# Kernel tuning notes

Measured on AMD Instinct MI355X. Metric: run time of the kernel, lower is better.

The kernel has to match this reference:

```python
import jax, jax.numpy as jnp
import numpy as np
import math

B, S, D = 2, 1024, 2048
NH, NKV, HD = 16, 8, 128
NREP = NH // NKV
WINDOW = 256  # = max_seq_len; ReRoPE window


def _rope(x, cos, sin):
    # x: (b, s, h, d); cos/sin broadcastable to (b, s, h, d//2). Interleaved pairs (llama2.c style).
    b, s, h, d = x.shape
    xr, xi = x[..., ::2], x[..., 1::2]
    or_ = xr * cos - xi * sin
    oi = xr * sin + xi * cos
    return jnp.stack([or_, oi], axis=-1).reshape(b, s, h, d)


def setup_inputs() -> dict:
    key = jax.random.key(0)
    kx, kq, kk, kv, ko = jax.random.split(key, 5)
    # real RoPE tables (theta=10000), per-position, half head dim
    inv = 1.0 / (10000.0 ** (np.arange(0, HD, 2, dtype=np.float32) / HD))
    fr = np.outer(np.arange(S, dtype=np.float32), inv).astype(np.float32)  # (S, HD//2)
    sc = 0.02
    return {
        "x": jax.random.normal(kx, (B, S, D), jnp.float32),
        "freqs_cos": jnp.asarray(np.cos(fr)),
        "freqs_sin": jnp.asarray(np.sin(fr)),
        "wq": jax.random.normal(kq, (D, NH * HD), jnp.float32) * sc,
        "wk": jax.random.normal(kk, (D, NKV * HD), jnp.float32) * sc,
        "wv": jax.random.normal(kv, (D, NKV * HD), jnp.float32) * sc,
        "wo": jax.random.normal(ko, (NH * HD, D), jnp.float32) * sc,
    }


def reference(x, freqs_cos, freqs_sin, wq, wk, wv, wo):
    b, s, _ = x.shape
    xq = (x @ wq).reshape(b, s, NH, HD)
    xk = (x @ wk).reshape(b, s, NKV, HD)
    xv = (x @ wv).reshape(b, s, NKV, HD)

    cos = freqs_cos[:s][None, :, None, :]
    sin = freqs_sin[:s][None, :, None, :]
    q1 = _rope(xq, cos, sin)   # standard RoPE
    k1 = _rope(xk, cos, sin)

    # ReRoPE: queries rotated at the fixed clamp position = window; keys unrotated
    cw = freqs_cos[WINDOW][None, None, None, :]
    sw = freqs_sin[WINDOW][None, None, None, :]
    q2 = _rope(xq, cw, sw)
    k2 = xk

    rep = lambda a: jnp.repeat(a, NREP, axis=2)          # repeat_kv (GQA)
    heads = lambda a: a.transpose(0, 2, 1, 3)            # (b, h, s, d)
    q1, k1, v = heads(q1), heads(rep(k1)), heads(rep(xv))
    q2, k2 = heads(q2), heads(rep(k2))

    scale = 1.0 / math.sqrt(HD)
    s1 = jnp.einsum("bhqd,bhkd->bhqk", q1, k1) * scale
    s2 = jnp.einsum("bhqd,bhkd->bhqk", q2, k2) * scale

    i = jnp.arange(s)[:, None]
    j = jnp.arange(s)[None, :]
    causal = j <= i
    rect = causal & (j > i - WINDOW)                     # rectified_mask band
    scores = jnp.where(rect, s1, s2)
    scores = jnp.where(causal, scores, -jnp.inf)         # mask_inf (causal)

    attn = jax.nn.softmax(scores.astype(jnp.float32), axis=-1).astype(x.dtype)
    out = jnp.einsum("bhqk,bhkd->bhqd", attn, v)
    out = out.transpose(0, 2, 1, 3).reshape(b, s, NH * HD)
    return out @ wo
```

## Files before the change

kernel.cpp:

```cpp
#include <hip/hip_runtime.h>
#include <hip/hip_bf16.h>

#define BDIM 2
#define SDIM 1024
#define DDIM 2048
#define NH 16
#define NKV 8
#define HD 128
#define WINDOW 256

typedef __bf16 bf16;
typedef __bf16 bf16x4 __attribute__((ext_vector_type(4)));
typedef __bf16 bf16x8 __attribute__((ext_vector_type(8)));
typedef float f32x4 __attribute__((ext_vector_type(4)));

#define L2E 1.44269504088896341f

__device__ inline bf16x8 load8(const bf16* p) { return *reinterpret_cast<const bf16x8*>(p); }

__device__ __forceinline__ void gl_lds16(const bf16* g, bf16* l) {
  __builtin_amdgcn_global_load_lds(
      (__attribute__((address_space(1))) void*)g,
      (__attribute__((address_space(3))) void*)l,
      16, 0, 0);
}

__global__ __launch_bounds__(256) void prep(const float* __restrict__ x,
                                            const float* __restrict__ wq,
                                            const float* __restrict__ wk,
                                            const float* __restrict__ wv,
                                            const float* __restrict__ wo,
                                            bf16* __restrict__ xb,
                                            bf16* __restrict__ wqkvT,
                                            bf16* __restrict__ woT) {
  __shared__ bf16 tile[32][33];
  int z = blockIdx.z;
  int tx = threadIdx.x, ty = threadIdx.y;
  if (z == 4) {
    long i = (((long)blockIdx.y * 64 + blockIdx.x) * 256 + ty * 32 + tx) * 4;
    float4 a = *(const float4*)(x + i);
    bf16x4 o;
    o[0] = (bf16)a.x; o[1] = (bf16)a.y; o[2] = (bf16)a.z; o[3] = (bf16)a.w;
    *(bf16x4*)(xb + i) = o;
    return;
  }
  const float* src; bf16* dst; int C;
  if (z == 0)      { src = wq; dst = wqkvT;                 C = 2048; }
  else if (z == 1) { src = wk; dst = wqkvT + 2048L * 2048;  C = 1024; }
  else if (z == 2) { src = wv; dst = wqkvT + 3072L * 2048;  C = 1024; }
  else             { src = wo; dst = woT;                   C = 2048; }
  int c0 = blockIdx.x * 32, r0 = blockIdx.y * 32;
  if (c0 >= C) return;
  for (int yy = ty; yy < 32; yy += 8)
    tile[yy][tx] = (bf16)src[(long)(r0 + yy) * C + c0 + tx];
  __syncthreads();
  for (int yy = ty; yy < 32; yy += 8)
    dst[(long)(c0 + yy) * 2048 + r0 + tx] = tile[tx][yy];
}

#define BK 64
__global__ __launch_bounds__(256) void gemm_bt_n64(const bf16* __restrict__ A,
                                                   const bf16* __restrict__ Bt,
                                                   float* __restrict__ C,
                                                   int M, int N, int K) {
  __shared__ bf16 smem[2 * 12288];
  int t = threadIdx.x;
  int wid = t >> 6, lane = t & 63;
  int wm = (wid >> 1) * 64, wn = (wid & 1) * 32;
  int fm = lane & 15, quad = lane >> 4;

  int wg = blockIdx.y * 32 + blockIdx.x;
  int swz = (wg & 7) * 64 + (wg >> 3);
  int by = swz >> 5, bx = swz & 31;
  int m0 = by * 128, n0 = bx * 64;

  const bf16* Ag = A + (long)m0 * K;
  const bf16* Bg = Bt + (long)n0 * K;

  f32x4 acc[4][2] = {};

  auto stA = [&](bf16* dst, int k0, int p) {
    int idx = p * 256 + t;
    int row = idx >> 3, ccs = idx & 7;
    int gcol = ((ccs ^ (row & 7)) * 8);
    gl_lds16(&Ag[(long)row * K + k0 + gcol], &dst[idx * 8]);
  };
  auto stB = [&](bf16* dst, int k0, int p) {
    int idx = p * 256 + t;
    int row = idx >> 3, ccs = idx & 7;
    int gcol = ((ccs ^ (row & 7)) * 8);
    gl_lds16(&Bg[(long)row * K + k0 + gcol], &dst[idx * 8]);
  };
  auto cmp = [&](const bf16* As, const bf16* Bs, int ks) {
    int cc = (ks >> 3) + quad;
    bf16x8 af[4], bfr[2];
    for (int i = 0; i < 4; ++i) {
      int fr = wm + i * 16 + fm;
      af[i] = load8(&As[(fr * 8 + (cc ^ (fr & 7))) * 8]);
    }
    for (int j = 0; j < 2; ++j) {
      int fr = wn + j * 16 + fm;
      bfr[j] = load8(&Bs[(fr * 8 + (cc ^ (fr & 7))) * 8]);
    }
    __builtin_amdgcn_s_setprio(1);
    for (int i = 0; i < 4; ++i)
      for (int j = 0; j < 2; ++j)
        acc[i][j] = __builtin_amdgcn_mfma_f32_16x16x32_bf16(af[i], bfr[j], acc[i][j], 0, 0, 0);
    __builtin_amdgcn_s_setprio(0);
  };

  {
    bf16* As = smem; bf16* Bs = smem + 8192;
    stA(As, 0, 0); stA(As, 0, 1); stA(As, 0, 2); stA(As, 0, 3);
    stB(Bs, 0, 0); stB(Bs, 0, 1);
  }
  const int NT = K / BK;
  for (int kt = 0; kt < NT; ++kt) {
    int cur = kt & 1;
    bf16* As = smem + cur * 12288;
    bf16* Bs = As + 8192;
    if (kt + 1 < NT) {
      bf16* An = smem + (cur ^ 1) * 12288;
      bf16* Bn = An + 8192;
      int kn = (kt + 1) * BK;
      stA(An, kn, 0); stA(An, kn, 1); stB(Bn, kn, 0);
      asm volatile("s_waitcnt vmcnt(3)\n\ts_barrier" ::: "memory");
      cmp(As, Bs, 0);
      stA(An, kn, 2); stA(An, kn, 3); stB(Bn, kn, 1);
      cmp(As, Bs, 32);
      asm volatile("s_barrier" ::: "memory");
    } else {
      asm volatile("s_waitcnt vmcnt(0)\n\ts_barrier" ::: "memory");
      cmp(As, Bs, 0);
      cmp(As, Bs, 32);
    }
  }
  for (int i = 0; i < 4; ++i)
    for (int r = 0; r < 4; ++r) {
      int row = m0 + wm + i * 16 + quad * 4 + r;
      for (int j = 0; j < 2; ++j) {
        int col = n0 + wn + j * 16 + fm;
        C[(long)row * N + col] = acc[i][j][r];
      }
    }
}

#define VPITCH 130
__global__ __launch_bounds__(512) void gemm_qkv(const bf16* __restrict__ A,
                                                const bf16* __restrict__ Bt,
                                                const float* __restrict__ fc,
                                                const float* __restrict__ fs,
                                                bf16* __restrict__ q0,
                                                bf16* __restrict__ k1,
                                                bf16* __restrict__ k2,
                                                bf16* __restrict__ vT) {
  const int K = 2048;
  __shared__ bf16 smem[2 * 24576];
  int t = threadIdx.x;
  int wid = t >> 6, lane = t & 63;
  int wm = (wid >> 2) * 64, wn = (wid & 3) * 64;
  int fm = lane & 15, quad = lane >> 4;

  int wg = blockIdx.y * 16 + blockIdx.x;
  int swz = (wg & 7) * 32 + (wg >> 3);
  int by = swz >> 4, bx = swz & 15;
  int m0 = by * 128, n0 = bx * 256;

  const bf16* Ag = A + (long)m0 * K;
  const bf16* Bg = Bt + (long)n0 * K;

  f32x4 acc[4][4] = {};

  auto stA = [&](bf16* dst, int k0, int p) {
    int idx = p * 512 + t;
    int row = idx >> 3, ccs = idx & 7;
    int gcol = ((ccs ^ (row & 7)) * 8);
    gl_lds16(&Ag[(long)row * K + k0 + gcol], &dst[idx * 8]);
  };
  auto stB = [&](bf16* dst, int k0, int p) {
    int idx = p * 512 + t;
    int row = idx >> 3, ccs = idx & 7;
    int gcol = ((ccs ^ (row & 7)) * 8);
    gl_lds16(&Bg[(long)row * K + k0 + gcol], &dst[idx * 8]);
  };
  auto cmp = [&](const bf16* As, const bf16* Bs, int ks) {
    int cc = (ks >> 3) + quad;
    bf16x8 af[4], bfr[4];
    for (int i = 0; i < 4; ++i) {
      int fr = wm + i * 16 + fm;
      af[i] = load8(&As[(fr * 8 + (cc ^ (fr & 7))) * 8]);
    }
    for (int j = 0; j < 4; ++j) {
      int fr = wn + j * 16 + fm;
      bfr[j] = load8(&Bs[(fr * 8 + (cc ^ (fr & 7))) * 8]);
    }
    __builtin_amdgcn_s_setprio(1);
    for (int i = 0; i < 4; ++i)
      for (int j = 0; j < 4; ++j)
        acc[i][j] = __builtin_amdgcn_mfma_f32_16x16x32_bf16(af[i], bfr[j], acc[i][j], 0, 0, 0);
    __builtin_amdgcn_s_setprio(0);
  };

  {
    bf16* As = smem; bf16* Bs = smem + 8192;
    stA(As, 0, 0); stA(As, 0, 1);
    stB(Bs, 0, 0); stB(Bs, 0, 1); stB(Bs, 0, 2); stB(Bs, 0, 3);
  }
  const int NT = K / 64;
  for (int kt = 0; kt < NT; ++kt) {
    int cur = kt & 1;
    bf16* As = smem + cur * 24576;
    bf16* Bs = As + 8192;
    if (kt + 1 < NT) {
      bf16* An = smem + (cur ^ 1) * 24576;
      bf16* Bn = An + 8192;
      int kn = (kt + 1) * 64;
      stA(An, kn, 0); stA(An, kn, 1); stB(Bn, kn, 0);
      asm volatile("s_waitcnt vmcnt(3)\n\ts_barrier" ::: "memory");
      cmp(As, Bs, 0);
      stB(Bn, kn, 1); stB(Bn, kn, 2); stB(Bn, kn, 3);
      cmp(As, Bs, 32);
      asm volatile("s_barrier" ::: "memory");
    } else {
      asm volatile("s_waitcnt vmcnt(0)\n\ts_barrier" ::: "memory");
      cmp(As, Bs, 0);
      cmp(As, Bs, 32);
    }
  }

  if (n0 < 2048) {
    const float scale = 0.08838834764831845f;
    for (int i = 0; i < 4; ++i)
      for (int r = 0; r < 4; ++r) {
        int row = m0 + wm + i * 16 + quad * 4 + r;
        for (int j = 0; j < 4; ++j) {
          int gc = n0 + wn + j * 16 + fm;
          q0[(long)row * 2048 + gc] = (bf16)(acc[i][j][r] * scale);
        }
      }
  } else if (n0 < 3072) {
    float sgn = (lane & 1) ? 1.f : -1.f;
    float cwj[4], swj[4];
    for (int j = 0; j < 4; ++j) {
      int dp = ((wn + j * 16 + fm) & 127) >> 1;
      cwj[j] = fc[WINDOW * 64 + dp];
      swj[j] = fs[WINDOW * 64 + dp] * (-sgn);
    }
    for (int i = 0; i < 4; ++i)
      for (int r = 0; r < 4; ++r) {
        int row = m0 + wm + i * 16 + quad * 4 + r;
        int s = row & (SDIM - 1);
        for (int j = 0; j < 4; ++j) {
          int kc = n0 - 2048 + wn + j * 16 + fm;
          int dp = (kc & 127) >> 1;
          float v = acc[i][j][r];
          float pp = __shfl_xor(v, 1, 64);
          float c = fc[s * 64 + dp];
          float sn = fs[s * 64 + dp] * sgn;
          long dst = (long)row * 1024 + kc;
          k1[dst] = (bf16)(v * c + pp * sn);
          k2[dst] = (bf16)(v * cwj[j] + pp * swj[j]);
        }
      }
  } else {
    int vv0 = (n0 - 3072) >> 7;
    int s0l = m0 & (SDIM - 1);
    int bq = m0 >> 10;
    for (int half = 0; half < 2; ++half) {
      __syncthreads();
      if (((wn >> 7) & 1) == half) {
        for (int i = 0; i < 4; ++i)
          for (int j = 0; j < 4; ++j) {
            int col = (wn & 127) + j * 16 + fm;
            for (int r = 0; r < 4; ++r) {
              int rl = wm + i * 16 + quad * 4 + r;
              smem[col * VPITCH + rl] = (bf16)acc[i][j][r];
            }
          }
      }
      __syncthreads();
      bf16* vtg = vT + ((long)(bq * NKV + vv0 + half)) * 128 * 1024;
      for (int p = 0; p < 4; ++p) {
        int c = p * 512 + t;
        int d = c >> 4, sc = (c & 15) * 8;
        *(bf16x8*)&vtg[(long)d * 1024 + s0l + sc] = *(bf16x8*)&smem[d * VPITCH + sc];
      }
    }
  }
}

__global__ __launch_bounds__(512) void attn_kernel(const bf16* __restrict__ q0,
                                                   const bf16* __restrict__ k1,
                                                   const bf16* __restrict__ k2,
                                                   const bf16* __restrict__ vT,
                                                   const float* __restrict__ fc,
                                                   const float* __restrict__ fs,
                                                   bf16* __restrict__ aout) {
  __shared__ bf16 Kb[3][8192];
  __shared__ bf16 Vb[3][8192];
  __shared__ bf16 Pl[8][16][72];
  __shared__ float stats[8][16];

  int kvh = blockIdx.y;
  int b = blockIdx.z;
  int tile = b ? (15 - blockIdx.x) : blockIdx.x;
  int t = threadIdx.x;
  int w = t >> 6, lane = t & 63;
  int wl = w & 3;
  int h = kvh * 2 + (w >> 2);
  int m = lane & 15, quad = lane >> 4;

  const bf16* k1g0 = k1 + ((long)b * SDIM) * 1024 + kvh * 128;
  const bf16* k2g0 = k2 + ((long)b * SDIM) * 1024 + kvh * 128;
  const bf16* vtg0 = vT + ((long)(b * NKV + kvh)) * 128 * 1024;

  int t0 = tile * 64;
  int i0w = t0 + wl * 16;
  int i = i0w + m;

  const bf16* q0p = q0 + ((long)(b * SDIM + i0w + m)) * 2048 + h * 128 + quad * 8;
  bf16x8 q0f[4], q1f[4];
  for (int kc = 0; kc < 4; ++kc) {
    q0f[kc] = load8(q0p + kc * 32);
    for (int p4 = 0; p4 < 4; ++p4) {
      int dp = kc * 16 + quad * 4 + p4;
      float c = fc[i * 64 + dp], sn = fs[i * 64 + dp];
      float xr = (float)q0f[kc][2 * p4], xi = (float)q0f[kc][2 * p4 + 1];
      q1f[kc][2 * p4]     = (bf16)(xr * c - xi * sn);
      q1f[kc][2 * p4 + 1] = (bf16)(xr * sn + xi * c);
    }
  }

  int NS2 = tile >= 4 ? tile - 3 : 0;
  int NSEG = NS2 + (tile < 4 ? tile + 1 : 5);
  int j1base = tile >= 4 ? t0 - 256 : 0;

  auto segj = [&](int s, int& j0, int& md) {
    if (s < NS2) { j0 = s * 64; md = 2; } else { j0 = j1base + (s - NS2) * 64; md = 1; }
  };
  auto stage = [&](int s) {
    int j0, md; segj(s, j0, md);
    const bf16* kg0 = (md == 1) ? k1g0 : k2g0;
    bf16* Kd = Kb[s % 3];
    bf16* Vd = Vb[s % 3];
    for (int p = 0; p < 2; ++p) {
      int idx = p * 512 + t;
      int kr = idx >> 4, kcs = idx & 15;
      int kg = (kcs ^ (kr & 15)) * 8;
      gl_lds16(&kg0[(long)(j0 + kr) * 1024 + kg], &Kd[idx * 8]);
      int vd = idx >> 3, vcs = idx & 7;
      int vg = (vcs ^ (vd & 7)) * 8;
      gl_lds16(&vtg0[(long)vd * 1024 + j0 + vg], &Vd[idx * 8]);
    }
  };

  f32x4 o[8] = {};
  float mrow = -INFINITY, lrow = 0.f;

  stage(0);
  if (NSEG > 1) stage(1);

  for (int s = 0; s < NSEG; ++s) {
    if (s + 2 < NSEG) {
      stage(s + 2);
      asm volatile("s_waitcnt vmcnt(8)\n\ts_barrier" ::: "memory");
    } else if (s + 1 < NSEG) {
      asm volatile("s_waitcnt vmcnt(4)\n\ts_barrier" ::: "memory");
    } else {
      asm volatile("s_waitcnt vmcnt(0)\n\ts_barrier" ::: "memory");
    }

    int j0, md; segj(s, j0, md);
    bool fullseg = (md == 2) && (s < NS2 - 1);
    const bf16* Ks = Kb[s % 3];
    const bf16* VTs = Vb[s % 3];

    f32x4 sc[4] = {};
    __builtin_amdgcn_s_setprio(1);
    if (md == 1) {
      for (int st = 0; st < 4; ++st)
        for (int kc = 0; kc < 4; ++kc) {
          int cc = kc * 4 + quad;
          sc[st] = __builtin_amdgcn_mfma_f32_16x16x32_bf16(
              load8(&Ks[((st * 16 + m) * 16 + (cc ^ m)) * 8]), q1f[kc], sc[st], 0, 0, 0);
        }
    } else {
      for (int st = 0; st < 4; ++st)
        for (int kc = 0; kc < 4; ++kc) {
          int cc = kc * 4 + quad;
          sc[st] = __builtin_amdgcn_mfma_f32_16x16x32_bf16(
              load8(&Ks[((st * 16 + m) * 16 + (cc ^ m)) * 8]), q0f[kc], sc[st], 0, 0, 0);
        }
    }
    __builtin_amdgcn_s_setprio(0);

    float sv[4][4];
    for (int st = 0; st < 4; ++st)
      for (int r = 0; r < 4; ++r) {
        float v = sc[st][r];
        if (!fullseg) {
          int j = j0 + st * 16 + quad * 4 + r;
          if (md == 1) {
            if (j > i || j <= i - WINDOW) v = -INFINITY;
          } else {
            if (j > i - WINDOW) v = -INFINITY;
          }
        }
        sv[st][r] = v;
      }

    float bm = -INFINITY;
    for (int st = 0; st < 4; ++st)
      for (int r = 0; r < 4; ++r) bm = fmaxf(bm, sv[st][r]);
    bm = fmaxf(bm, __shfl_xor(bm, 16, 64));
    bm = fmaxf(bm, __shfl_xor(bm, 32, 64));
    float mnew = fmaxf(mrow, bm);
    float rs = 0.f;
    for (int st = 0; st < 4; ++st) {
      bf16x4 pk;
      for (int r = 0; r < 4; ++r) {
        float pvv = exp2f((sv[st][r] - mnew) * L2E);
        rs += pvv;
        pk[r] = (bf16)pvv;
      }
      *(bf16x4*)&Pl[w][m][st * 16 + quad * 4] = pk;
    }
    rs += __shfl_xor(rs, 16, 64);
    rs += __shfl_xor(rs, 32, 64);
    if (__any(mnew > mrow)) {
      float alpha = exp2f((mrow - mnew) * L2E);
      lrow = lrow * alpha + rs;
      mrow = mnew;
      if (lane < 16) stats[w][lane] = alpha;
      f32x4 av = *(f32x4*)&stats[w][quad * 4];
      for (int n8 = 0; n8 < 8; ++n8)
        for (int r = 0; r < 4; ++r) o[n8][r] *= av[r];
    } else {
      lrow += rs;
    }

    for (int kc = 0; kc < 2; ++kc) {
      bf16x8 af = load8(&Pl[w][m][kc * 32 + quad * 8]);
      int cc = kc * 4 + quad;
      __builtin_amdgcn_s_setprio(1);
      for (int n8 = 0; n8 < 8; ++n8) {
        int d = n8 * 16 + m;
        o[n8] = __builtin_amdgcn_mfma_f32_16x16x32_bf16(
            af, load8(&VTs[(d * 8 + (cc ^ (d & 7))) * 8]), o[n8], 0, 0, 0);
      }
      __builtin_amdgcn_s_setprio(0);
    }
    asm volatile("s_barrier" ::: "memory");
  }

  if (lane < 16) stats[w][lane] = lrow;
  __builtin_amdgcn_s_waitcnt(0);
  f32x4 lv = *(f32x4*)&stats[w][quad * 4];
  for (int n8 = 0; n8 < 8; ++n8)
    for (int r = 0; r < 4; ++r) {
      int row = i0w + quad * 4 + r;
      float val = o[n8][r] / lv[r];
      aout[((long)(b * SDIM + row)) * 2048 + h * 128 + n8 * 16 + m] = (bf16)val;
    }
}

extern "C" void kernel_launch(void* const* d_in, const int* in_sizes, int n_in,
                              void* d_out, int out_size, void* d_ws, size_t ws_size,
                              hipStream_t stream) {
  const float* x  = (const float*)d_in[0];
  const float* fc = (const float*)d_in[1];
  const float* fs = (const float*)d_in[2];
  const float* wq = (const float*)d_in[3];
  const float* wk = (const float*)d_in[4];
  const float* wv = (const float*)d_in[5];
  const float* wo = (const float*)d_in[6];
  float* out = (float*)d_out;

  bf16* wqkvT = (bf16*)d_ws;
  bf16* woT   = wqkvT + 4096L * 2048;
  bf16* xb    = woT + 2048L * 2048;
  bf16* q0b   = xb + 2048L * 2048;
  bf16* k1b   = q0b + 2048L * 2048;
  bf16* k2b   = k1b + 2048L * 1024;
  bf16* vT    = k2b + 2048L * 1024;
  bf16* aout  = vT + 2048L * 1024;

  prep<<<dim3(64, 64, 5), dim3(32, 8), 0, stream>>>(x, wq, wk, wv, wo, xb, wqkvT, woT);

  gemm_qkv<<<dim3(16, 16), 512, 0, stream>>>(xb, wqkvT, fc, fs, q0b, k1b, k2b, vT);

  attn_kernel<<<dim3(16, 8, 2), 512, 0, stream>>>(q0b, k1b, k2b, vT, fc, fs, aout);

  gemm_bt_n64<<<dim3(32, 16), 256, 0, stream>>>(aout, woT, out, 2048, 2048, 2048);
}
```

Measured before the change: 229.1 us.

## Restructure attention into 128-thread blocks with two query subtiles per wave

The attention kernel now runs 512 blocks of 2 waves, one wave per query head of the GQA pair. Each block covers 32 query rows, so each wave handles two 16-row subtiles that share the K and V fragment loads. The K/V pipeline drops from triple to double buffering, with a single barrier per segment. The mask-free segment test now also covers interior window segments. The aim is more blocks for better CU occupancy and load balance, plus more MFMA work per LDS load. The cost is more total K/V global traffic, because each 32-row tile restages its segments, and more register pressure from the doubled accumulators.

```diff
diff --git a/kernel.cpp b/kernel.cpp
--- a/kernel.cpp
+++ b/kernel.cpp
@@ -289,178 +289,227 @@
   }
 }
 
-__global__ __launch_bounds__(512) void attn_kernel(const bf16* __restrict__ q0,
+__global__ __launch_bounds__(128) void attn_kernel(const bf16* __restrict__ q0,
                                                    const bf16* __restrict__ k1,
                                                    const bf16* __restrict__ k2,
                                                    const bf16* __restrict__ vT,
                                                    const float* __restrict__ fc,
                                                    const float* __restrict__ fs,
                                                    bf16* __restrict__ aout) {
-  __shared__ bf16 Kb[3][8192];
-  __shared__ bf16 Vb[3][8192];
-  __shared__ bf16 Pl[8][16][72];
-  __shared__ float stats[8][16];
-
-  int kvh = blockIdx.y;
-  int b = blockIdx.z;
-  int tile = b ? (15 - blockIdx.x) : blockIdx.x;
+  __shared__ bf16 Kb[2][8192];
+  __shared__ bf16 Vb[2][8192];
+  __shared__ bf16 Pl[2][2][16][72];
+  __shared__ float stats[2][2][16];
+
+  int g = blockIdx.x;
+  int half = blockIdx.y;
+  int combo = g >> 4;
+  int kvh = combo & 7;
+  int b = combo >> 3;
+  int xt = g & 15;
+  int tile = half ? (31 - xt) : xt;
+
   int t = threadIdx.x;
   int w = t >> 6, lane = t & 63;
-  int wl = w & 3;
-  int h = kvh * 2 + (w >> 2);
+  int h = kvh * 2 + w;
   int m = lane & 15, quad = lane >> 4;
 
   const bf16* k1g0 = k1 + ((long)b * SDIM) * 1024 + kvh * 128;
   const bf16* k2g0 = k2 + ((long)b * SDIM) * 1024 + kvh * 128;
   const bf16* vtg0 = vT + ((long)(b * NKV + kvh)) * 128 * 1024;
 
-  int t0 = tile * 64;
-  int i0w = t0 + wl * 16;
-  int i = i0w + m;
-
-  const bf16* q0p = q0 + ((long)(b * SDIM + i0w + m)) * 2048 + h * 128 + quad * 8;
-  bf16x8 q0f[4], q1f[4];
-  for (int kc = 0; kc < 4; ++kc) {
-    q0f[kc] = load8(q0p + kc * 32);
-    for (int p4 = 0; p4 < 4; ++p4) {
-      int dp = kc * 16 + quad * 4 + p4;
-      float c = fc[i * 64 + dp], sn = fs[i * 64 + dp];
-      float xr = (float)q0f[kc][2 * p4], xi = (float)q0f[kc][2 * p4 + 1];
-      q1f[kc][2 * p4]     = (bf16)(xr * c - xi * sn);
-      q1f[kc][2 * p4 + 1] = (bf16)(xr * sn + xi * c);
-    }
-  }
-
-  int NS2 = tile >= 4 ? tile - 3 : 0;
-  int NSEG = NS2 + (tile < 4 ? tile + 1 : 5);
-  int j1base = tile >= 4 ? t0 - 256 : 0;
+  int t0 = tile * 32;
+  int i0w = t0;
+  int i0 = t0 + m;
+  int i1 = i0 + 16;
+
+  bf16x8 q0f[2][4], q1f[2][4];
+#pragma unroll
+  for (int ss = 0; ss < 2; ++ss) {
+    int isr = t0 + ss * 16 + m;
+    const bf16* q0p = q0 + ((long)(b * SDIM + isr)) * 2048 + h * 128 + quad * 8;
+#pragma unroll
+    for (int kc = 0; kc < 4; ++kc) {
+      q0f[ss][kc] = load8(q0p + kc * 32);
+#pragma unroll
+      for (int p4 = 0; p4 < 4; ++p4) {
+        int dp = kc * 16 + quad * 4 + p4;
+        float c = fc[isr * 64 + dp], sn = fs[isr * 64 + dp];
+        float xr = (float)q0f[ss][kc][2 * p4], xi = (float)q0f[ss][kc][2 * p4 + 1];
+        q1f[ss][kc][2 * p4]     = (bf16)(xr * c - xi * sn);
+        q1f[ss][kc][2 * p4 + 1] = (bf16)(xr * sn + xi * c);
+      }
+    }
+  }
+
+  int NS2 = (t0 >= 256) ? (((t0 - 225) >> 6) + 1) : 0;
+  int wb0 = (t0 >= 256) ? ((t0 - 255) >> 6) : 0;
+  int wend = (t0 + 31) >> 6;
+  int NSEG = NS2 + (wend - wb0 + 1);
+  int j1base = wb0 << 6;
 
   auto segj = [&](int s, int& j0, int& md) {
-    if (s < NS2) { j0 = s * 64; md = 2; } else { j0 = j1base + (s - NS2) * 64; md = 1; }
+    if (s < NS2) { j0 = s << 6; md = 2; } else { j0 = j1base + ((s - NS2) << 6); md = 1; }
   };
   auto stage = [&](int s) {
     int j0, md; segj(s, j0, md);
     const bf16* kg0 = (md == 1) ? k1g0 : k2g0;
-    bf16* Kd = Kb[s % 3];
-    bf16* Vd = Vb[s % 3];
-    for (int p = 0; p < 2; ++p) {
-      int idx = p * 512 + t;
+    bf16* Kd = Kb[s & 1];
+    bf16* Vd = Vb[s & 1];
+    for (int p = 0; p < 8; ++p) {
+      int idx = p * 128 + t;
       int kr = idx >> 4, kcs = idx & 15;
-      int kg = (kcs ^ (kr & 15)) * 8;
-      gl_lds16(&kg0[(long)(j0 + kr) * 1024 + kg], &Kd[idx * 8]);
+      gl_lds16(&kg0[(long)(j0 + kr) * 1024 + ((kcs ^ (kr & 15)) * 8)], &Kd[idx * 8]);
       int vd = idx >> 3, vcs = idx & 7;
-      int vg = (vcs ^ (vd & 7)) * 8;
-      gl_lds16(&vtg0[(long)vd * 1024 + j0 + vg], &Vd[idx * 8]);
-    }
-  };
-
-  f32x4 o[8] = {};
-  float mrow = -INFINITY, lrow = 0.f;
+      gl_lds16(&vtg0[(long)vd * 1024 + j0 + ((vcs ^ (vd & 7)) * 8)], &Vd[idx * 8]);
+    }
+  };
+
+  f32x4 o0[8] = {}, o1[8] = {};
+  float mrow0 = -INFINITY, lrow0 = 0.f;
+  float mrow1 = -INFINITY, lrow1 = 0.f;
 
   stage(0);
-  if (NSEG > 1) stage(1);
-
   for (int s = 0; s < NSEG; ++s) {
-    if (s + 2 < NSEG) {
-      stage(s + 2);
-      asm volatile("s_waitcnt vmcnt(8)\n\ts_barrier" ::: "memory");
-    } else if (s + 1 < NSEG) {
-      asm volatile("s_waitcnt vmcnt(4)\n\ts_barrier" ::: "memory");
-    } else {
-      asm volatile("s_waitcnt vmcnt(0)\n\ts_barrier" ::: "memory");
-    }
+    asm volatile("s_waitcnt vmcnt(0)" ::: "memory");
+    __builtin_amdgcn_s_barrier();
+    if (s + 1 < NSEG) stage(s + 1);
 
     int j0, md; segj(s, j0, md);
-    bool fullseg = (md == 2) && (s < NS2 - 1);
-    const bf16* Ks = Kb[s % 3];
-    const bf16* VTs = Vb[s % 3];
-
-    f32x4 sc[4] = {};
+    const bf16* Ks = Kb[s & 1];
+    const bf16* VTs = Vb[s & 1];
+
+    f32x4 sc0[4] = {}, sc1[4] = {};
     __builtin_amdgcn_s_setprio(1);
     if (md == 1) {
+#pragma unroll
       for (int st = 0; st < 4; ++st)
+#pragma unroll
         for (int kc = 0; kc < 4; ++kc) {
           int cc = kc * 4 + quad;
-          sc[st] = __builtin_amdgcn_mfma_f32_16x16x32_bf16(
-              load8(&Ks[((st * 16 + m) * 16 + (cc ^ m)) * 8]), q1f[kc], sc[st], 0, 0, 0);
+          bf16x8 kf = load8(&Ks[((st * 16 + m) * 16 + (cc ^ m)) * 8]);
+          sc0[st] = __builtin_amdgcn_mfma_f32_16x16x32_bf16(kf, q1f[0][kc], sc0[st], 0, 0, 0);
+          sc1[st] = __builtin_amdgcn_mfma_f32_16x16x32_bf16(kf, q1f[1][kc], sc1[st], 0, 0, 0);
         }
     } else {
+#pragma unroll
       for (int st = 0; st < 4; ++st)
+#pragma unroll
         for (int kc = 0; kc < 4; ++kc) {
           int cc = kc * 4 + quad;
-          sc[st] = __builtin_amdgcn_mfma_f32_16x16x32_bf16(
-              load8(&Ks[((st * 16 + m) * 16 + (cc ^ m)) * 8]), q0f[kc], sc[st], 0, 0, 0);
+          bf16x8 kf = load8(&Ks[((st * 16 + m) * 16 + (cc ^ m)) * 8]);
+          sc0[st] = __builtin_amdgcn_mfma_f32_16x16x32_bf16(kf, q0f[0][kc], sc0[st], 0, 0, 0);
+          sc1[st] = __builtin_amdgcn_mfma_f32_16x16x32_bf16(kf, q0f[1][kc], sc1[st], 0, 0, 0);
         }
     }
     __builtin_amdgcn_s_setprio(0);
 
-    float sv[4][4];
+    bool fullseg = (md == 2) ? (s < NS2 - 1)
+                             : ((j0 >= t0 - 224) && (j0 <= t0 - 64));
+    float sv0[4][4], sv1[4][4];
     for (int st = 0; st < 4; ++st)
       for (int r = 0; r < 4; ++r) {
-        float v = sc[st][r];
+        float v0 = sc0[st][r], v1 = sc1[st][r];
         if (!fullseg) {
           int j = j0 + st * 16 + quad * 4 + r;
           if (md == 1) {
-            if (j > i || j <= i - WINDOW) v = -INFINITY;
+            if (j > i0 || j <= i0 - WINDOW) v0 = -INFINITY;
+            if (j > i1 || j <= i1 - WINDOW) v1 = -INFINITY;
           } else {
-            if (j > i - WINDOW) v = -INFINITY;
+            if (j > i0 - WINDOW) v0 = -INFINITY;
+            if (j > i1 - WINDOW) v1 = -INFINITY;
           }
         }
-        sv[st][r] = v;
-      }
-
-    float bm = -INFINITY;
+        sv0[st][r] = v0; sv1[st][r] = v1;
+      }
+
+    float bm0 = -INFINITY;
     for (int st = 0; st < 4; ++st)
-      for (int r = 0; r < 4; ++r) bm = fmaxf(bm, sv[st][r]);
-    bm = fmaxf(bm, __shfl_xor(bm, 16, 64));
-    bm = fmaxf(bm, __shfl_xor(bm, 32, 64));
-    float mnew = fmaxf(mrow, bm);
-    float rs = 0.f;
+      for (int r = 0; r < 4; ++r) bm0 = fmaxf(bm0, sv0[st][r]);
+    bm0 = fmaxf(bm0, __shfl_xor(bm0, 16, 64));
+    bm0 = fmaxf(bm0, __shfl_xor(bm0, 32, 64));
+    float mnew0 = fmaxf(mrow0, bm0);
+    float rs0 = 0.f;
     for (int st = 0; st < 4; ++st) {
       bf16x4 pk;
       for (int r = 0; r < 4; ++r) {
-        float pvv = exp2f((sv[st][r] - mnew) * L2E);
-        rs += pvv;
+        float pvv = exp2f((sv0[st][r] - mnew0) * L2E);
+        rs0 += pvv;
         pk[r] = (bf16)pvv;
       }
-      *(bf16x4*)&Pl[w][m][st * 16 + quad * 4] = pk;
-    }
-    rs += __shfl_xor(rs, 16, 64);
-    rs += __shfl_xor(rs, 32, 64);
-    if (__any(mnew > mrow)) {
-      float alpha = exp2f((mrow - mnew) * L2E);
-      lrow = lrow * alpha + rs;
-      mrow = mnew;
-      if (lane < 16) stats[w][lane] = alpha;
-      f32x4 av = *(f32x4*)&stats[w][quad * 4];
+      *(bf16x4*)&Pl[w][0][m][st * 16 + quad * 4] = pk;
+    }
+    rs0 += __shfl_xor(rs0, 16, 64);
+    rs0 += __shfl_xor(rs0, 32, 64);
+    if (__any(mnew0 > mrow0)) {
+      float alpha = exp2f((mrow0 - mnew0) * L2E);
+      lrow0 = lrow0 * alpha + rs0;
+      mrow0 = mnew0;
+      if (lane < 16) stats[w][0][lane] = alpha;
+      f32x4 av = *(f32x4*)&stats[w][0][quad * 4];
       for (int n8 = 0; n8 < 8; ++n8)
-        for (int r = 0; r < 4; ++r) o[n8][r] *= av[r];
+        for (int r = 0; r < 4; ++r) o0[n8][r] *= av[r];
     } else {
-      lrow += rs;
-    }
-
+      lrow0 += rs0;
+    }
+
+    float bm1 = -INFINITY;
+    for (int st = 0; st < 4; ++st)
+      for (int r = 0; r < 4; ++r) bm1 = fmaxf(bm1, sv1[st][r]);
+    bm1 = fmaxf(bm1, __shfl_xor(bm1, 16, 64));
+    bm1 = fmaxf(bm1, __shfl_xor(bm1, 32, 64));
+    float mnew1 = fmaxf(mrow1, bm1);
+    float rs1 = 0.f;
+    for (int st = 0; st < 4; ++st) {
+      bf16x4 pk;
+      for (int r = 0; r < 4; ++r) {
+        float pvv = exp2f((sv1[st][r] - mnew1) * L2E);
+        rs1 += pvv;
+        pk[r] = (bf16)pvv;
+      }
+      *(bf16x4*)&Pl[w][1][m][st * 16 + quad * 4] = pk;
+    }
+    rs1 += __shfl_xor(rs1, 16, 64);
+    rs1 += __shfl_xor(rs1, 32, 64);
+    if (__any(mnew1 > mrow1)) {
+      float alpha = exp2f((mrow1 - mnew1) * L2E);
+      lrow1 = lrow1 * alpha + rs1;
+      mrow1 = mnew1;
+      if (lane < 16) stats[w][1][lane] = alpha;
+      f32x4 av = *(f32x4*)&stats[w][1][quad * 4];
+      for (int n8 = 0; n8 < 8; ++n8)
+        for (int r = 0; r < 4; ++r) o1[n8][r] *= av[r];
+    } else {
+      lrow1 += rs1;
+    }
+
+#pragma unroll
     for (int kc = 0; kc < 2; ++kc) {
-      bf16x8 af = load8(&Pl[w][m][kc * 32 + quad * 8]);
+      bf16x8 af0 = load8(&Pl[w][0][m][kc * 32 + quad * 8]);
+      bf16x8 af1 = load8(&Pl[w][1][m][kc * 32 + quad * 8]);
       int cc = kc * 4 + quad;
       __builtin_amdgcn_s_setprio(1);
+#pragma unroll
       for (int n8 = 0; n8 < 8; ++n8) {
         int d = n8 * 16 + m;
-        o[n8] = __builtin_amdgcn_mfma_f32_16x16x32_bf16(
-            af, load8(&VTs[(d * 8 + (cc ^ (d & 7))) * 8]), o[n8], 0, 0, 0);
+        bf16x8 vf = load8(&VTs[(d * 8 + (cc ^ (d & 7))) * 8]);
+        o0[n8] = __builtin_amdgcn_mfma_f32_16x16x32_bf16(af0, vf, o0[n8], 0, 0, 0);
+        o1[n8] = __builtin_amdgcn_mfma_f32_16x16x32_bf16(af1, vf, o1[n8], 0, 0, 0);
       }
       __builtin_amdgcn_s_setprio(0);
     }
-    asm volatile("s_barrier" ::: "memory");
-  }
-
-  if (lane < 16) stats[w][lane] = lrow;
+  }
+
+  if (lane < 16) { stats[w][0][lane] = lrow0; stats[w][1][lane] = lrow1; }
   __builtin_amdgcn_s_waitcnt(0);
-  f32x4 lv = *(f32x4*)&stats[w][quad * 4];
+  f32x4 lv0 = *(f32x4*)&stats[w][0][quad * 4];
+  f32x4 lv1 = *(f32x4*)&stats[w][1][quad * 4];
   for (int n8 = 0; n8 < 8; ++n8)
     for (int r = 0; r < 4; ++r) {
-      int row = i0w + quad * 4 + r;
-      float val = o[n8][r] / lv[r];
-      aout[((long)(b * SDIM + row)) * 2048 + h * 128 + n8 * 16 + m] = (bf16)val;
+      int row0 = t0 + quad * 4 + r;
+      aout[((long)(b * SDIM + row0)) * 2048 + h * 128 + n8 * 16 + m] = (bf16)(o0[n8][r] / lv0[r]);
+      int row1 = row0 + 16;
+      aout[((long)(b * SDIM + row1)) * 2048 + h * 128 + n8 * 16 + m] = (bf16)(o1[n8][r] / lv1[r]);
     }
 }
 
@@ -489,7 +538,7 @@
 
   gemm_qkv<<<dim3(16, 16), 512, 0, stream>>>(xb, wqkvT, fc, fs, q0b, k1b, k2b, vT);
 
-  attn_kernel<<<dim3(16, 8, 2), 512, 0, stream>>>(q0b, k1b, k2b, vT, fc, fs, aout);
+  attn_kernel<<<dim3(256, 2, 1), 128, 0, stream>>>(q0b, k1b, k2b, vT, fc, fs, aout);
 
   gemm_bt_n64<<<dim3(32, 16), 256, 0, stream>>>(aout, woT, out, 2048, 2048, 2048);
 }
```

New measurement: 246.5 us. 7.6% more time.
